# Performance work log

Measured on AMD Instinct MI355X. Metric: run time of the kernel, lower is better.

## Reference

```python
import jax, jax.numpy as jnp
import numpy as np

EPS = 1e-8
NUM_LAYERS = 6


def setup_inputs() -> dict:
    key = jax.random.key(0)
    ks = jax.random.split(key, 8)
    N, Cin, Cout, S, H, W = 4, 256, 256, 512, 64, 64
    fan_in = Cin  # kaiming for 1x1 conv, leaky_relu a=0 -> gain sqrt(2)
    return {
        "x": jax.random.normal(ks[0], (N, Cin, H, W), dtype=jnp.float32),
        "y": jax.random.normal(ks[1], (N, S), dtype=jnp.float32),
        "ch_conv_w": jax.random.normal(ks[2], (Cout, Cin), dtype=jnp.float32) / np.sqrt(fan_in),
        "ch_conv_b": jnp.zeros((Cout,), dtype=jnp.float32),
        "affine_w": jax.random.normal(ks[3], (NUM_LAYERS, Cout, S), dtype=jnp.float32) / np.sqrt(S),
        "affine_b": jnp.zeros((NUM_LAYERS, Cout), dtype=jnp.float32),
        "mod_w": jax.random.normal(ks[4], (NUM_LAYERS, Cout, Cout), dtype=jnp.float32) * np.sqrt(2.0 / Cout),
    }


def _forward(x, y, ch_conv_w, ch_conv_b, affine_w, affine_b, mod_w):
    # 1x1 channel conv (with bias)
    x = jnp.einsum("oi,bihw->bohw", ch_conv_w, x) + ch_conv_b[None, :, None, None]
    x = jnp.repeat(jnp.repeat(x, 2, axis=2), 2, axis=3)
    # channel repeat_interleave(2) -> [N, 2C, H, W]
    x = jnp.repeat(x, 2, axis=1)

    C = x.shape[1] // 2
    for i in range(NUM_LAYERS):
        x1, x2 = x[:, :C], x[:, C:]
        # SpatialShift2d with default directions pads [1,1,1,1] (replicate) then
        # crops the identical region for every split -> exact identity.
        y1 = x1 + x2
        # g-branch: Conv2dMod(k=1) with per-sample style modulation + exact GELU
        s = jnp.einsum("cs,bs->bc", affine_w[i], y) + affine_b[i]  # [B, C]
        wmod = mod_w[i][None] * (s[:, :, None] + 1.0)              # [B, O, I] (style scales OUTPUT channel)
        d = jax.lax.rsqrt(jnp.sum(wmod * wmod, axis=2, keepdims=True) + EPS)
        wmod = wmod * d
        h = jnp.einsum("boi,bihw->bohw", wmod, y1)
        y2 = x2 + jax.nn.gelu(h, approximate=False)
        x = jnp.concatenate([y1, y2], axis=1)

    x1, x2 = x[:, :C], x[:, C:]
    return (x1 + x2) * 0.5


def reference(x, y, ch_conv_w, ch_conv_b, affine_w, affine_b, mod_w):
    return _forward(x, y, ch_conv_w, ch_conv_b, affine_w, affine_b, mod_w)
```

## Files before the change

kernel.cpp:

```cpp
#include <hip/hip_runtime.h>
#include <math.h>

#define NB 4
#define CC 256
#define SS 512
#define NL 6
#define SLOT_HW 65536

typedef __attribute__((ext_vector_type(8))) short s16x8;
typedef __attribute__((ext_vector_type(4))) float f32x4;
typedef __attribute__((ext_vector_type(2))) float f32x2;
typedef __attribute__((ext_vector_type(4))) unsigned short u16x4;

__device__ __forceinline__ unsigned short f2bf(float f) {
    unsigned u = __builtin_bit_cast(unsigned, f);
    u += 0x7FFFu + ((u >> 16) & 1u);
    return (unsigned short)(u >> 16);
}
__device__ __forceinline__ float gelu_fast(float x) {
    float u = x * (1.0f + 0.044715f * x * x);
    float e = __expf(-1.5957691216f * u);
    return x * __builtin_amdgcn_rcpf(1.0f + e);
}


__global__ __launch_bounds__(256) void prep_kernel(
    const float* __restrict__ y, const float* __restrict__ aw,
    const float* __restrict__ ab, const float* __restrict__ mw,
    const float* __restrict__ cw, unsigned short* __restrict__ wsBF)
{
    int w = threadIdx.x >> 6, lane = threadIdx.x & 63;

    if (blockIdx.x >= 1536) {
        int m = (blockIdx.x - 1536)*4 + w;
#pragma unroll
        for (int u = 0; u < 4; ++u) {
            int k = lane + 64*u;
            int f = (m >> 4)*8 + (k >> 5);
            int hw = f*512 + ((k >> 3) & 3)*128 + (m & 15)*8 + (k & 7);
            wsBF[hw] = f2bf(cw[(size_t)m*CC + k]);
        }
        return;
    }

    int r = blockIdx.x*4 + w;
    int l = r >> 10;
    int b = (r >> 8) & 3;
    int o = r & 255;

    const float* awr = aw + (size_t)(l*CC + o)*SS;
    const float* yb  = y + (size_t)b*SS;
    float s = 0.f;
#pragma unroll
    for (int j = 0; j < 8; ++j) { int idx = lane + 64*j; s += awr[idx]*yb[idx]; }
#pragma unroll
    for (int off = 32; off; off >>= 1) s += __shfl_xor(s, off);
    float t = s + ab[l*CC + o] + 1.0f;

    const float* mwr = mw + (size_t)(l*CC + o)*CC;
    float wv[4]; float ss = 0.f;
#pragma unroll
    for (int u = 0; u < 4; ++u) { int j = lane + 64*u; wv[u] = mwr[j]*t; ss += wv[u]*wv[u]; }
#pragma unroll
    for (int off = 32; off; off >>= 1) ss += __shfl_xor(ss, off);
    float d = 1.0f / sqrtf(ss + 1e-8f);

    unsigned short* slot = wsBF + (size_t)(1 + l*NB + b)*SLOT_HW;
#pragma unroll
    for (int u = 0; u < 4; ++u) {
        int k = lane + 64*u;
        int f = (o >> 4)*8 + (k >> 5);
        int hw = f*512 + ((k >> 3) & 3)*128 + (o & 15)*8 + (k & 7);
        slot[hw] = f2bf(wv[u]*d);
    }
}

#define BFRAGL(buf, kq, nt, kcl) \
    (lds + (buf)*16384 + ((((kq)*2 + (nt))*2 + (kcl)))*1024)

__global__ __launch_bounds__(512, 4) void fused_kernel(
    const float* __restrict__ x, const float* __restrict__ cb,
    const unsigned short* __restrict__ wsBF, float* __restrict__ out)
{
    __shared__ __align__(16) unsigned char lds[69632];
    float* xS = (float*)(lds + 32768);
    float* S2 = (float*)(lds + 32768);

    const int tid  = threadIdx.x;
    const int lane = tid & 63;
    const int w    = tid >> 6;
    const int l15  = lane & 15;
    const int q    = lane >> 4;

    const int bswz  = blockIdx.x & 7;
    const int b     = bswz >> 1;
    const int half  = bswz & 1;
    const int strip = blockIdx.x >> 3;
    const int n0    = strip * 64 + half * 32;

    float y1[2][2][4], y2[2][2][4];
    f32x4 acc[2][2];

#pragma unroll
    for (int t = 0; t < 2; ++t)
#pragma unroll
        for (int s = 0; s < 2; ++s) acc[t][s] = 0;

    {
#pragma unroll
        for (int p = 0; p < 4; ++p) {
            int row = (tid >> 3) + 64*p, c4 = (tid & 7) * 4;
            float4 v = *(const float4*)&x[((size_t)(b*CC + row))*4096 + n0 + c4];
            *(float4*)&xS[row*36 + c4] = v;
        }
    }
    __syncthreads();
    {
        int n = tid & 31, k0 = (tid >> 5) * 16;
        int nt = n >> 4, n15 = n & 15;
#pragma unroll
        for (int j = 0; j < 4; ++j) {
            int k = k0 + 4*j;
            u16x4 hv;
#pragma unroll
            for (int i = 0; i < 4; ++i) hv[i] = f2bf(xS[(k+i)*36 + n]);
            int kq = k >> 6, kcl = (k >> 5) & 1, qq = (k >> 3) & 3, jb = k & 7;
            *(u16x4*)(BFRAGL(0,kq,nt,kcl) + (16*qq + n15)*16 + jb*2) = hv;
        }
    }
    {
        const unsigned short* slot = wsBF;
        s16x8 aS[8][2];
#pragma unroll
        for (int p = 0; p < 4; ++p)
#pragma unroll
        for (int t = 0; t < 2; ++t)
            aS[p][t] = *(const s16x8*)(slot + (size_t)(((2*w+t)*8 + p)*512) + lane*8);
        __syncthreads();
#pragma unroll
        for (int step = 0; step < 8; ++step) {
            if (step < 4) {
#pragma unroll
                for (int t = 0; t < 2; ++t)
                    aS[step+4][t] = *(const s16x8*)(slot + (size_t)(((2*w+t)*8 + step+4)*512) + lane*8);
            }
            int kq = step >> 1, kcl = step & 1;
#pragma unroll
            for (int s = 0; s < 2; ++s) {
                s16x8 bh = *(const s16x8*)(BFRAGL(0,kq,s,kcl) + lane*16);
#pragma unroll
                for (int t = 0; t < 2; ++t)
                    acc[t][s] = __builtin_amdgcn_mfma_f32_16x16x32_bf16(aS[step][t], bh, acc[t][s], 0, 0, 0);
            }
        }
    }

#pragma unroll
    for (int pass = 0; pass < 2; ++pass) {
        __syncthreads();
        if ((w >> 2) == pass) {
#pragma unroll
            for (int t = 0; t < 2; ++t)
#pragma unroll
            for (int s = 0; s < 2; ++s)
#pragma unroll
            for (int r = 0; r < 4; ++r) {
                int m  = 32*w + 16*t + 4*q + r;
                int nl = 16*s + l15;
                S2[(m - 128*pass)*33 + nl] = acc[t][s][r] + cb[m];
            }
        }
        __syncthreads();
#pragma unroll
        for (int t = 0; t < 2; ++t)
#pragma unroll
        for (int s = 0; s < 2; ++s)
#pragma unroll
        for (int r = 0; r < 4; ++r) {
            int c  = 32*w + 16*t + 4*q + r;
            int nl = 16*s + l15;
            float v = S2[(c >> 1)*33 + nl];
            if (pass == 0) { y1[t][s][r] = v; }
            else           { y2[t][s][r] = v; y1[t][s][r] += v; }
        }
    }

    for (int l = 0; l < NL; ++l) {
        const int buf = l & 1;
        const unsigned short* slot = wsBF + (size_t)(1 + l*NB + b)*SLOT_HW;
#pragma unroll
        for (int t = 0; t < 2; ++t)
#pragma unroll
            for (int s = 0; s < 2; ++s) acc[t][s] = 0;

        {
            int kq = w >> 1, kcl = w & 1, jb = 4*(q & 1);
#pragma unroll
            for (int t = 0; t < 2; ++t) {
                int qq = 2*t + (q >> 1);
#pragma unroll
                for (int s = 0; s < 2; ++s) {
                    u16x4 hv;
#pragma unroll
                    for (int r = 0; r < 4; ++r) hv[r] = f2bf(y1[t][s][r]);
                    *(u16x4*)(BFRAGL(buf,kq,s,kcl) + (16*qq + l15)*16 + jb*2) = hv;
                }
            }
        }
        s16x8 aS[8][2];
#pragma unroll
        for (int p = 0; p < 4; ++p)
#pragma unroll
        for (int t = 0; t < 2; ++t)
            aS[p][t] = *(const s16x8*)(slot + (size_t)(((2*w+t)*8 + p)*512) + lane*8);
        __syncthreads();
#pragma unroll
        for (int step = 0; step < 8; ++step) {
            if (step < 4) {
#pragma unroll
                for (int t = 0; t < 2; ++t)
                    aS[step+4][t] = *(const s16x8*)(slot + (size_t)(((2*w+t)*8 + step+4)*512) + lane*8);
            }
            int kq = step >> 1, kcl = step & 1;
#pragma unroll
            for (int s = 0; s < 2; ++s) {
                s16x8 bh = *(const s16x8*)(BFRAGL(buf,kq,s,kcl) + lane*16);
#pragma unroll
                for (int t = 0; t < 2; ++t)
                    acc[t][s] = __builtin_amdgcn_mfma_f32_16x16x32_bf16(aS[step][t], bh, acc[t][s], 0, 0, 0);
            }
        }
#pragma unroll
        for (int t = 0; t < 2; ++t)
#pragma unroll
        for (int s = 0; s < 2; ++s)
#pragma unroll
        for (int r = 0; r < 4; ++r) {
            y2[t][s][r] += gelu_fast(acc[t][s][r]);
            if (l < NL - 1) y1[t][s][r] += y2[t][s][r];
        }
    }

#pragma unroll
    for (int t = 0; t < 2; ++t)
#pragma unroll
    for (int s = 0; s < 2; ++s)
#pragma unroll
    for (int r = 0; r < 4; ++r) {
        int ch  = 32*w + 16*t + 4*q + r;
        int wpx = half*32 + 16*s + l15;
        float v = 0.5f*(y1[t][s][r] + y2[t][s][r]);
        f32x2 vv = {v, v};
        size_t base = (((size_t)(b*CC + ch)*128 + 2*strip))*128 + 2*wpx;
        __builtin_nontemporal_store(vv, (f32x2*)&out[base]);
        __builtin_nontemporal_store(vv, (f32x2*)&out[base + 128]);
    }
}

extern "C" void kernel_launch(void* const* d_in, const int* in_sizes, int n_in,
                              void* d_out, int out_size, void* d_ws, size_t ws_size,
                              hipStream_t stream) {
    const float* x  = (const float*)d_in[0];
    const float* y  = (const float*)d_in[1];
    const float* cw = (const float*)d_in[2];
    const float* cb = (const float*)d_in[3];
    const float* aw = (const float*)d_in[4];
    const float* ab = (const float*)d_in[5];
    const float* mw = (const float*)d_in[6];
    float* out = (float*)d_out;

    unsigned short* wsBF = (unsigned short*)d_ws;

    prep_kernel<<<1600, 256, 0, stream>>>(y, aw, ab, mw, cw, wsBF);
    fused_kernel<<<512, 512, 0, stream>>>(x, cb, wsBF, out);
}
```

Measured before the change: 119.1 us.

## Merge weight prep into main kernel with grid barrier and factored modulation

Removes the separate prep kernel and does the weight conversion and style computation inside the main kernel before a grid-wide atomic barrier. Modulation is factored algebraically: the per-sample output-channel scale and demodulation become a per-(layer,batch,channel) scalar applied to the matmul result. This lets all batches share one bf16 weight slot per layer instead of one per batch. It removes a kernel launch and shrinks the prep work, but adds a memset, a spin barrier that requires all 512 blocks to be co-resident, and an extra multiply per accumulator.

```diff
diff --git a/kernel.cpp b/kernel.cpp
--- a/kernel.cpp
+++ b/kernel.cpp
@@ -6,6 +6,8 @@
 #define SS 512
 #define NL 6
 #define SLOT_HW 65536
+#define G_OFF_HW   (7*SLOT_HW)
+#define CTR_BYTE   942080
 
 typedef __attribute__((ext_vector_type(8))) short s16x8;
 typedef __attribute__((ext_vector_type(4))) float f32x4;
@@ -24,67 +26,20 @@
 }
 
 
-__global__ __launch_bounds__(256) void prep_kernel(
-    const float* __restrict__ y, const float* __restrict__ aw,
-    const float* __restrict__ ab, const float* __restrict__ mw,
-    const float* __restrict__ cw, unsigned short* __restrict__ wsBF)
-{
-    int w = threadIdx.x >> 6, lane = threadIdx.x & 63;
-
-    if (blockIdx.x >= 1536) {
-        int m = (blockIdx.x - 1536)*4 + w;
-#pragma unroll
-        for (int u = 0; u < 4; ++u) {
-            int k = lane + 64*u;
-            int f = (m >> 4)*8 + (k >> 5);
-            int hw = f*512 + ((k >> 3) & 3)*128 + (m & 15)*8 + (k & 7);
-            wsBF[hw] = f2bf(cw[(size_t)m*CC + k]);
-        }
-        return;
-    }
-
-    int r = blockIdx.x*4 + w;
-    int l = r >> 10;
-    int b = (r >> 8) & 3;
-    int o = r & 255;
-
-    const float* awr = aw + (size_t)(l*CC + o)*SS;
-    const float* yb  = y + (size_t)b*SS;
-    float s = 0.f;
-#pragma unroll
-    for (int j = 0; j < 8; ++j) { int idx = lane + 64*j; s += awr[idx]*yb[idx]; }
-#pragma unroll
-    for (int off = 32; off; off >>= 1) s += __shfl_xor(s, off);
-    float t = s + ab[l*CC + o] + 1.0f;
-
-    const float* mwr = mw + (size_t)(l*CC + o)*CC;
-    float wv[4]; float ss = 0.f;
-#pragma unroll
-    for (int u = 0; u < 4; ++u) { int j = lane + 64*u; wv[u] = mwr[j]*t; ss += wv[u]*wv[u]; }
-#pragma unroll
-    for (int off = 32; off; off >>= 1) ss += __shfl_xor(ss, off);
-    float d = 1.0f / sqrtf(ss + 1e-8f);
-
-    unsigned short* slot = wsBF + (size_t)(1 + l*NB + b)*SLOT_HW;
-#pragma unroll
-    for (int u = 0; u < 4; ++u) {
-        int k = lane + 64*u;
-        int f = (o >> 4)*8 + (k >> 5);
-        int hw = f*512 + ((k >> 3) & 3)*128 + (o & 15)*8 + (k & 7);
-        slot[hw] = f2bf(wv[u]*d);
-    }
-}
-
 #define BFRAGL(buf, kq, nt, kcl) \
     (lds + (buf)*16384 + ((((kq)*2 + (nt))*2 + (kcl)))*1024)
 
-__global__ __launch_bounds__(512, 4) void fused_kernel(
-    const float* __restrict__ x, const float* __restrict__ cb,
-    const unsigned short* __restrict__ wsBF, float* __restrict__ out)
+__global__ __launch_bounds__(512, 4) void mono_kernel(
+    const float* __restrict__ x, const float* __restrict__ y,
+    const float* __restrict__ cw, const float* __restrict__ cb,
+    const float* __restrict__ aw, const float* __restrict__ ab,
+    const float* __restrict__ mw, unsigned short* __restrict__ wsBF,
+    unsigned int* __restrict__ ctr, float* __restrict__ out)
 {
     __shared__ __align__(16) unsigned char lds[69632];
     float* xS = (float*)(lds + 32768);
     float* S2 = (float*)(lds + 32768);
+    float* gtab = (float*)(wsBF + G_OFF_HW);
 
     const int tid  = threadIdx.x;
     const int lane = tid & 63;
@@ -101,18 +56,50 @@
     float y1[2][2][4], y2[2][2][4];
     f32x4 acc[2][2];
 
-#pragma unroll
-    for (int t = 0; t < 2; ++t)
-#pragma unroll
-        for (int s = 0; s < 2; ++s) acc[t][s] = 0;
-
-    {
-#pragma unroll
-        for (int p = 0; p < 4; ++p) {
-            int row = (tid >> 3) + 64*p, c4 = (tid & 7) * 4;
-            float4 v = *(const float4*)&x[((size_t)(b*CC + row))*4096 + n0 + c4];
-            *(float4*)&xS[row*36 + c4] = v;
-        }
+    float4 xr[4];
+#pragma unroll
+    for (int p = 0; p < 4; ++p) {
+        int row = (tid >> 3) + 64*p, c4 = (tid & 7) * 4;
+        xr[p] = *(const float4*)&x[((size_t)(b*CC + row))*4096 + n0 + c4];
+    }
+    if (blockIdx.x < 224) {
+        int row = blockIdx.x*8 + w;
+        int sl  = row >> 8, m = row & 255;
+        const float* src = (sl == 0) ? (cw + (size_t)m*CC)
+                                     : (mw + ((size_t)(sl-1)*CC + m)*CC);
+        unsigned short* dst = wsBF + (size_t)sl*SLOT_HW;
+#pragma unroll
+        for (int u = 0; u < 4; ++u) {
+            int k = lane + 64*u;
+            int f = (m >> 4)*8 + (k >> 5);
+            int hw = f*512 + ((k >> 3) & 3)*128 + (m & 15)*8 + (k & 7);
+            dst[hw] = f2bf(src[k]);
+        }
+    }
+    for (int rr = w; rr < 12; rr += 8) {
+        int r  = blockIdx.x*12 + rr;
+        int pl = r >> 10, pb = (r >> 8) & 3, po = r & 255;
+        const float* awr = aw + (size_t)(pl*CC + po)*SS;
+        const float* yb  = y + (size_t)pb*SS;
+        float s = 0.f;
+#pragma unroll
+        for (int j = 0; j < 8; ++j) { int idx = lane + 64*j; s += awr[idx]*yb[idx]; }
+        const float* mwr = mw + ((size_t)pl*CC + po)*CC;
+        float qs = 0.f;
+#pragma unroll
+        for (int u = 0; u < 4; ++u) { float v = mwr[lane + 64*u]; qs += v*v; }
+#pragma unroll
+        for (int off = 32; off; off >>= 1) {
+            s  += __shfl_xor(s, off);
+            qs += __shfl_xor(qs, off);
+        }
+        float t = s + ab[pl*CC + po] + 1.0f;
+        if (lane == 0) gtab[r] = t * (1.0f / sqrtf(t*t*qs + 1e-8f));
+    }
+#pragma unroll
+    for (int p = 0; p < 4; ++p) {
+        int row = (tid >> 3) + 64*p, c4 = (tid & 7) * 4;
+        *(float4*)&xS[row*36 + c4] = xr[p];
     }
     __syncthreads();
     {
@@ -128,6 +115,21 @@
             *(u16x4*)(BFRAGL(0,kq,nt,kcl) + (16*qq + n15)*16 + jb*2) = hv;
         }
     }
+    __threadfence();
+    __syncthreads();
+    if (tid == 0) {
+        __hip_atomic_fetch_add(ctr, 1u, __ATOMIC_ACQ_REL, __HIP_MEMORY_SCOPE_AGENT);
+        while (__hip_atomic_load(ctr, __ATOMIC_ACQUIRE, __HIP_MEMORY_SCOPE_AGENT) < 512u)
+            __builtin_amdgcn_s_sleep(2);
+    }
+    __syncthreads();
+    __threadfence();
+
+#pragma unroll
+    for (int t = 0; t < 2; ++t)
+#pragma unroll
+        for (int s = 0; s < 2; ++s) acc[t][s] = 0;
+
     {
         const unsigned short* slot = wsBF;
         s16x8 aS[8][2];
@@ -136,7 +138,6 @@
 #pragma unroll
         for (int t = 0; t < 2; ++t)
             aS[p][t] = *(const s16x8*)(slot + (size_t)(((2*w+t)*8 + p)*512) + lane*8);
-        __syncthreads();
 #pragma unroll
         for (int step = 0; step < 8; ++step) {
             if (step < 4) {
@@ -187,7 +188,7 @@
 
     for (int l = 0; l < NL; ++l) {
         const int buf = l & 1;
-        const unsigned short* slot = wsBF + (size_t)(1 + l*NB + b)*SLOT_HW;
+        const unsigned short* slot = wsBF + (size_t)(1 + l)*SLOT_HW;
 #pragma unroll
         for (int t = 0; t < 2; ++t)
 #pragma unroll
@@ -213,6 +214,12 @@
 #pragma unroll
         for (int t = 0; t < 2; ++t)
             aS[p][t] = *(const s16x8*)(slot + (size_t)(((2*w+t)*8 + p)*512) + lane*8);
+        float gv[2][4];
+#pragma unroll
+        for (int t = 0; t < 2; ++t)
+#pragma unroll
+        for (int r = 0; r < 4; ++r)
+            gv[t][r] = gtab[l*1024 + b*256 + 32*w + 16*t + 4*q + r];
         __syncthreads();
 #pragma unroll
         for (int step = 0; step < 8; ++step) {
@@ -236,7 +243,7 @@
         for (int s = 0; s < 2; ++s)
 #pragma unroll
         for (int r = 0; r < 4; ++r) {
-            y2[t][s][r] += gelu_fast(acc[t][s][r]);
+            y2[t][s][r] += gelu_fast(acc[t][s][r] * gv[t][r]);
             if (l < NL - 1) y1[t][s][r] += y2[t][s][r];
         }
     }
@@ -270,7 +277,8 @@
     float* out = (float*)d_out;
 
     unsigned short* wsBF = (unsigned short*)d_ws;
-
-    prep_kernel<<<1600, 256, 0, stream>>>(y, aw, ab, mw, cw, wsBF);
-    fused_kernel<<<512, 512, 0, stream>>>(x, cb, wsBF, out);
-}
+    unsigned int* ctr = (unsigned int*)((char*)d_ws + CTR_BYTE);
+
+    hipMemsetAsync(ctr, 0, 64, stream);
+    mono_kernel<<<512, 512, 0, stream>>>(x, y, cw, cb, aw, ab, mw, wsBF, ctr, out);
+}
```

Result: slower. 265.3 us (+122.8%).
